# Performance work log

Measured on AMD Instinct MI355X. Metric: run time of the kernel, lower is better.

The kernel has to match this reference:

```python
import jax, jax.numpy as jnp
import numpy as np

# dims: batch, seq, state_dim, hidden, action_dim, layers, heads, bucket_size
B, T, SD, C, A, L, H, BS = 4, 4096, 256, 1024, 64, 6, 16, 64
HD = C // H
SCALE = 1.0 / np.sqrt(HD).astype(np.float32)
EPS = 1e-5


def _ln(x, w, b):
    m = jnp.mean(x, axis=-1, keepdims=True)
    v = jnp.var(x, axis=-1, keepdims=True)
    return (x - m) * jax.lax.rsqrt(v + EPS) * w + b


def _attn(x, qkv_w, qkv_b, out_w, out_b):
    # bucketed local attention: each bucket attends to itself + previous bucket (causal within own bucket)
    Bx, Tx, Cx = x.shape
    nb = Tx // BS
    qkv = x @ qkv_w + qkv_b                              # [B,T,3C]
    q, k, v = jnp.split(qkv, 3, axis=-1)
    bkt = lambda t: t.reshape(Bx, nb, BS, H, HD).transpose(0, 1, 3, 2, 4)  # [B,nb,H,BS,HD]
    qb, kb, vb = bkt(q), bkt(k), bkt(v)
    # previous bucket (first bucket's 'previous' is zeros), matching torch.roll + zeroing bucket 0
    kp = jnp.concatenate([jnp.zeros_like(kb[:, :1]), kb[:, :-1]], axis=1)
    vp = jnp.concatenate([jnp.zeros_like(vb[:, :1]), vb[:, :-1]], axis=1)
    kc = jnp.concatenate([kp, kb], axis=3)               # [B,nb,H,2BS,HD]
    vc = jnp.concatenate([vp, vb], axis=3)
    s = jnp.einsum('bnhid,bnhjd->bnhij', qb, kc) * SCALE # [B,nb,H,BS,2BS]
    i = jnp.arange(BS)[:, None]
    j = jnp.arange(2 * BS)[None, :]
    mask = (j < BS) | (j - BS <= i)
    s = jnp.where(mask, s, -jnp.inf)
    a = jax.nn.softmax(s, axis=-1)
    o = jnp.einsum('bnhij,bnhjd->bnhid', a, vc)          # [B,nb,H,BS,HD]
    o = o.transpose(0, 1, 3, 2, 4).reshape(Bx, Tx, Cx)
    return o @ out_w + out_b


def setup_inputs() -> dict:
    key = jax.random.key(0)
    ks = iter(jax.random.split(key, 40))
    rn = lambda shape, std=0.02: jax.random.normal(next(ks), shape, jnp.float32) * std
    return {
        'states': jax.random.normal(next(ks), (B, T, SD), jnp.float32),
        'state_embed_w': rn((SD, C)),
        'state_embed_b': jnp.zeros((C,), jnp.float32),
        'pos_embed': rn((1, T, C)),
        'ln1_w': jnp.ones((L, C), jnp.float32),
        'ln1_b': jnp.zeros((L, C), jnp.float32),
        'qkv_w': rn((L, C, 3 * C)),
        'qkv_b': jnp.zeros((L, 3 * C), jnp.float32),
        'attn_out_w': rn((L, C, C)),
        'attn_out_b': jnp.zeros((L, C), jnp.float32),
        'ln2_w': jnp.ones((L, C), jnp.float32),
        'ln2_b': jnp.zeros((L, C), jnp.float32),
        'mlp_w1': rn((L, C, 4 * C)),
        'mlp_b1': jnp.zeros((L, 4 * C), jnp.float32),
        'mlp_w2': rn((L, 4 * C, C)),
        'mlp_b2': jnp.zeros((L, C), jnp.float32),
        'lnf_w': jnp.ones((C,), jnp.float32),
        'lnf_b': jnp.zeros((C,), jnp.float32),
        'actor_w': rn((C, A)),
        'actor_b': jnp.zeros((A,), jnp.float32),
        'actor_logstd': jnp.zeros((1, A), jnp.float32),
        'critic_w': rn((C, 1)),
        'critic_b': jnp.zeros((1,), jnp.float32),
    }


def reference(states, state_embed_w, state_embed_b, pos_embed,
              ln1_w, ln1_b, qkv_w, qkv_b, attn_out_w, attn_out_b,
              ln2_w, ln2_b, mlp_w1, mlp_b1, mlp_w2, mlp_b2,
              lnf_w, lnf_b, actor_w, actor_b, actor_logstd, critic_w, critic_b):
    x = states @ state_embed_w + state_embed_b + pos_embed[:, :T]

    def step(x, p):
        l1w, l1b, qw, qb, ow, ob, l2w, l2b, w1, b1, w2, b2 = p
        x = x + _attn(_ln(x, l1w, l1b), qw, qb, ow, ob)
        h = _ln(x, l2w, l2b)
        x = x + (jax.nn.gelu(h @ w1 + b1, approximate=False) @ w2 + b2)
        return x, None

    blocks = (ln1_w, ln1_b, qkv_w, qkv_b, attn_out_w, attn_out_b,
              ln2_w, ln2_b, mlp_w1, mlp_b1, mlp_w2, mlp_b2)
    x, _ = jax.lax.scan(step, x, blocks)
    x = _ln(x, lnf_w, lnf_b)
    logits = x @ actor_w + actor_b          # [B,T,A]
    values = x @ critic_w + critic_b        # [B,T,1]
    return (logits, actor_logstd, values)
```

## Files before the change

### kernel.cpp

```cpp
#include <hip/hip_runtime.h>
#include <math.h>
#include <stdint.h>

#define T_SEQ 4096
#define CDIM  1024
#define NL    6
#define NH    16
#define BSZ   64
#define HDIM  64
#define MROWS 16384

typedef __bf16 bf16x8 __attribute__((ext_vector_type(8)));
typedef float  f32x4  __attribute__((ext_vector_type(4)));

__device__ __forceinline__ unsigned short f2bf(float f) {
  __bf16 h = (__bf16)f;
  return __builtin_bit_cast(unsigned short, h);
}
__device__ __forceinline__ float bf2f(unsigned short u) {
  unsigned int v = ((unsigned int)u) << 16;
  return __builtin_bit_cast(float, v);
}

typedef __attribute__((address_space(3))) unsigned int* lds_u32p;
typedef const __attribute__((address_space(1))) unsigned int* glb_u32p;
__device__ __forceinline__ void glds16(const void* g, void* l) {
  __builtin_amdgcn_global_load_lds((glb_u32p)(uintptr_t)g, (lds_u32p)(uintptr_t)l, 16, 0, 0);
}

__device__ __forceinline__ float erf_fast(float x) {
  float ax = fabsf(x);
  float t = __builtin_amdgcn_rcpf(fmaf(0.3275911f, ax, 1.0f));
  float y = t * fmaf(t, fmaf(t, fmaf(t, fmaf(t, 1.061405429f, -1.453152027f),
                                     1.421413741f), -0.284496736f), 0.254829592f);
  float r = 1.0f - y * __expf(-ax * ax);
  return copysignf(r, x);
}
__device__ __forceinline__ float gelu_fast(float v) {
  return 0.5f * v * (1.0f + erf_fast(v * 0.70710678118654752440f));
}

template<int OBF>
__global__ __launch_bounds__(256) void ln_kernel(const float* __restrict__ x,
    const float* __restrict__ w, const float* __restrict__ bb, void* __restrict__ out)
{
  int row = blockIdx.x;
  int tid = threadIdx.x;
  float4 v = ((const float4*)(x + (size_t)row * CDIM))[tid];
  float s  = v.x + v.y + v.z + v.w;
  float ss = v.x*v.x + v.y*v.y + v.z*v.z + v.w*v.w;
  #pragma unroll
  for (int o = 32; o > 0; o >>= 1) { s += __shfl_down(s, o); ss += __shfl_down(ss, o); }
  __shared__ float red[8];
  int wid = tid >> 6, lane = tid & 63;
  if (lane == 0) { red[wid] = s; red[4 + wid] = ss; }
  __syncthreads();
  if (tid == 0) {
    red[0] = red[0] + red[1] + red[2] + red[3];
    red[4] = red[4] + red[5] + red[6] + red[7];
  }
  __syncthreads();
  float mean = red[0] * (1.0f / CDIM);
  float var  = red[4] * (1.0f / CDIM) - mean * mean;
  float inv  = 1.0f / sqrtf(var + 1e-5f);
  float4 w4 = ((const float4*)w)[tid];
  float4 b4 = ((const float4*)bb)[tid];
  float4 o4;
  o4.x = (v.x - mean) * inv * w4.x + b4.x;
  o4.y = (v.y - mean) * inv * w4.y + b4.y;
  o4.z = (v.z - mean) * inv * w4.z + b4.z;
  o4.w = (v.w - mean) * inv * w4.w + b4.w;
  if (OBF) {
    ushort4 o;
    o.x = f2bf(o4.x); o.y = f2bf(o4.y); o.z = f2bf(o4.z); o.w = f2bf(o4.w);
    ((ushort4*)((unsigned short*)out + (size_t)row * CDIM))[tid] = o;
  } else {
    ((float4*)((float*)out + (size_t)row * CDIM))[tid] = o4;
  }
}

__global__ __launch_bounds__(256) void convT(const float* __restrict__ W,
    unsigned short* __restrict__ Wt, int K, int N)
{
  __shared__ float tile[32][33];
  const int kt = blockIdx.y * 32, nt = blockIdx.x * 32;
  const int r = threadIdx.x >> 3;
  const int c = (threadIdx.x & 7) * 4;
  float4 v = *(const float4*)(W + (size_t)(kt + r) * N + nt + c);
  tile[r][c] = v.x; tile[r][c+1] = v.y; tile[r][c+2] = v.z; tile[r][c+3] = v.w;
  __syncthreads();
  ushort4 o;
  o.x = f2bf(tile[c+0][r]); o.y = f2bf(tile[c+1][r]);
  o.z = f2bf(tile[c+2][r]); o.w = f2bf(tile[c+3][r]);
  *(ushort4*)(Wt + (size_t)(nt + r) * K + kt + c) = o;
}

__global__ void conv_flat(const float* __restrict__ in, unsigned short* __restrict__ out)
{
  int i = blockIdx.x * blockDim.x + threadIdx.x;
  float4 v = ((const float4*)in)[i];
  ushort4 o;
  o.x = f2bf(v.x); o.y = f2bf(v.y); o.z = f2bf(v.z); o.w = f2bf(v.w);
  ((ushort4*)out)[i] = o;
}

#define EPAD 68
#define GTILE 65536
template<int EPI, int OBF>
__global__ __launch_bounds__(512, 2) void gemm_bf16(
    const unsigned short* __restrict__ A, const unsigned short* __restrict__ Bt,
    const float* __restrict__ bias, const float* __restrict__ extra,
    void* __restrict__ Cout, int M, int N, int K)
{
  __shared__ __align__(16) char smem[2 * GTILE];
  const int tid = threadIdx.x;
  const int wave = tid >> 6, lane = tid & 63;
  const int ln15 = lane & 15, quad = lane >> 4;

  const int ntiles = N >> 8;
  const int per = ntiles << 3;
  const int g = blockIdx.x / per, rr = blockIdx.x % per;
  const int m0 = ((g << 3) + (rr & 7)) << 8;
  const int n0 = (rr >> 3) << 8;
  const int wm = (wave >> 2) * 128, wn = (wave & 3) * 64;

  const int srow = lane >> 3;
  const int scol = ((lane & 7) ^ srow) << 4;
  const size_t rs = (size_t)K * 2;
  const char* aSrc = (const char*)(A + (size_t)(m0 + wave * 8 + srow) * K) + scol;
  const char* bSrc = (const char*)(Bt + (size_t)(n0 + wave * 8 + srow) * K) + scol;
  const int sdst = wave * 1024;

  const int axor = (ln15 & 7) << 4;
  const int kq0 = (quad * 16) ^ axor;
  const int kq1 = (64 + quad * 16) ^ axor;
  const int aRd = (wm + ln15) * 128;
  const int bRd = (wn + ln15) * 128;

  f32x4 acc[8][4];
  #pragma unroll
  for (int i = 0; i < 8; ++i)
    #pragma unroll
    for (int j = 0; j < 4; ++j) acc[i][j] = (f32x4){0.f, 0.f, 0.f, 0.f};

  bf16x8 af[4][2];
  bf16x8 bfr[4][2];

  #define STAGE_A(buf, kt2) { \
    const char* s_ = aSrc + (size_t)(kt2) * 128; \
    char* d_ = smem + (buf) * GTILE + sdst; \
    glds16(s_,             d_); \
    glds16(s_ +  64 * rs,  d_ + 8192); \
    glds16(s_ + 128 * rs,  d_ + 16384); \
    glds16(s_ + 192 * rs,  d_ + 24576); }
  #define STAGE_B(buf, kt2) { \
    const char* s_ = bSrc + (size_t)(kt2) * 128; \
    char* d_ = smem + (buf) * GTILE + 32768 + sdst; \
    glds16(s_,             d_); \
    glds16(s_ +  64 * rs,  d_ + 8192); \
    glds16(s_ + 128 * rs,  d_ + 16384); \
    glds16(s_ + 192 * rs,  d_ + 24576); }
  #define LDA(buf, mh) { \
    const char* p_ = smem + (buf) * GTILE + aRd + (mh) * 8192; \
    _Pragma("unroll") \
    for (int mf = 0; mf < 4; ++mf) { \
      af[mf][0] = *(const bf16x8*)(p_ + mf * 2048 + kq0); \
      af[mf][1] = *(const bf16x8*)(p_ + mf * 2048 + kq1); } }
  #define LDB(buf, nh) { \
    const char* p_ = smem + (buf) * GTILE + 32768 + bRd + (nh) * 4096; \
    _Pragma("unroll") \
    for (int nf = 0; nf < 2; ++nf) { \
      bfr[(nh)*2+nf][0] = *(const bf16x8*)(p_ + nf * 2048 + kq0); \
      bfr[(nh)*2+nf][1] = *(const bf16x8*)(p_ + nf * 2048 + kq1); } }
  #define MMA(mh, nh) { \
    _Pragma("unroll") \
    for (int mf = 0; mf < 4; ++mf) \
      _Pragma("unroll") \
      for (int nf = 0; nf < 2; ++nf) { \
        acc[(mh)*4+mf][(nh)*2+nf] = __builtin_amdgcn_mfma_f32_16x16x32_bf16( \
            af[mf][0], bfr[(nh)*2+nf][0], acc[(mh)*4+mf][(nh)*2+nf], 0, 0, 0); \
        acc[(mh)*4+mf][(nh)*2+nf] = __builtin_amdgcn_mfma_f32_16x16x32_bf16( \
            af[mf][1], bfr[(nh)*2+nf][1], acc[(mh)*4+mf][(nh)*2+nf], 0, 0, 0); } }
  #define WAIT_LGKM do { asm volatile("s_waitcnt lgkmcnt(0)" ::: "memory"); \
                         __builtin_amdgcn_sched_barrier(0); } while (0)

  const int KT = K >> 6;
  STAGE_A(0, 0); STAGE_B(0, 0);
  asm volatile("s_waitcnt vmcnt(0)" ::: "memory");
  __builtin_amdgcn_s_barrier();

  int cur = 0;
  for (int kt = 0; kt < KT; ++kt) {
    const int nxt = cur ^ 1;
    const bool pf = (kt + 1 < KT);
    LDA(cur, 0); LDB(cur, 0);
    if (pf) STAGE_A(nxt, kt + 1);
    __builtin_amdgcn_s_barrier();
    WAIT_LGKM;
    __builtin_amdgcn_s_setprio(1);
    MMA(0, 0);
    __builtin_amdgcn_s_setprio(0);
    __builtin_amdgcn_s_barrier();
    LDB(cur, 1);
    if (pf) STAGE_B(nxt, kt + 1);
    __builtin_amdgcn_s_barrier();
    WAIT_LGKM;
    __builtin_amdgcn_s_setprio(1);
    MMA(0, 1);
    __builtin_amdgcn_s_setprio(0);
    __builtin_amdgcn_s_barrier();
    LDA(cur, 1);
    __builtin_amdgcn_s_barrier();
    WAIT_LGKM;
    __builtin_amdgcn_s_setprio(1);
    MMA(1, 0);
    __builtin_amdgcn_s_setprio(0);
    __builtin_amdgcn_s_barrier();
    __builtin_amdgcn_s_setprio(1);
    MMA(1, 1);
    __builtin_amdgcn_s_setprio(0);
    asm volatile("s_waitcnt vmcnt(0)" ::: "memory");
    __builtin_amdgcn_s_barrier();
    cur = nxt;
  }

  __builtin_amdgcn_s_barrier();
  float* ep = (float*)smem + wave * 16 * EPAD;
  const int cl = ln15, rq = quad * 4;
  #pragma unroll
  for (int i = 0; i < 8; ++i) {
    #pragma unroll
    for (int j = 0; j < 4; ++j) {
      const float bj = bias[n0 + wn + j * 16 + cl];
      #pragma unroll
      for (int r = 0; r < 4; ++r) {
        float val = acc[i][j][r] + bj;
        if (EPI == 2) val = gelu_fast(val);
        if (OBF) ((unsigned short*)ep)[(rq + r) * (2 * EPAD) + j * 16 + cl] = f2bf(val);
        else     ep[(rq + r) * EPAD + j * 16 + cl] = val;
      }
    }
    const int mbase = m0 + wm + i * 16;
    if (OBF) {
      #pragma unroll
      for (int s = 0; s < 2; ++s) {
        int f = s * 64 + lane;
        int row = f >> 3, ch = f & 7;
        uint4 v = *(const uint4*)((const unsigned short*)ep + row * (2 * EPAD) + ch * 8);
        *(uint4*)((unsigned short*)Cout + (size_t)(mbase + row) * N + n0 + wn + ch * 8) = v;
      }
    } else {
      #pragma unroll
      for (int s = 0; s < 4; ++s) {
        int f = s * 64 + lane;
        int row = f >> 4, ch = f & 15;
        float4 v = *(const float4*)(ep + row * EPAD + ch * 4);
        const int m = mbase + row;
        const size_t off = (size_t)m * N + n0 + wn + ch * 4;
        if (EPI == 1) {
          float4 e = *(const float4*)(extra + off);
          v.x += e.x; v.y += e.y; v.z += e.z; v.w += e.w;
        } else if (EPI == 3) {
          float4 e = *(const float4*)(extra + (size_t)(m & (T_SEQ - 1)) * N + n0 + wn + ch * 4);
          v.x += e.x; v.y += e.y; v.z += e.z; v.w += e.w;
        }
        *(float4*)((float*)Cout + off) = v;
      }
    }
  }
  #undef STAGE_A
  #undef STAGE_B
  #undef LDA
  #undef LDB
  #undef MMA
  #undef WAIT_LGKM
}

template<int EPI>
__global__ __launch_bounds__(256) void gemm_f32(const float* __restrict__ A,
    const float* __restrict__ B, const float* __restrict__ bias,
    const float* __restrict__ extra, float* __restrict__ C,
    int M, int N, int K)
{
  __shared__ float As[16][64];
  __shared__ float Bs[16][64];
  const int tid = threadIdx.x;
  const int m0 = blockIdx.x * 64, n0 = blockIdx.y * 64;
  const int tx = tid & 15, ty = tid >> 4;
  const int ar = tid >> 2, ak = (tid & 3) * 4;
  const int br = tid >> 4, bc = (tid & 15) * 4;
  const float* Ap = A + (size_t)(m0 + ar) * K + ak;
  const float* Bp = B + (size_t)br * N + n0 + bc;
  float acc[4][4] = {};
  for (int k0 = 0; k0 < K; k0 += 16) {
    float4 av = *(const float4*)(Ap + k0);
    float4 bv = *(const float4*)(Bp + (size_t)k0 * N);
    __syncthreads();
    As[ak+0][ar] = av.x; As[ak+1][ar] = av.y; As[ak+2][ar] = av.z; As[ak+3][ar] = av.w;
    *(float4*)&Bs[br][bc] = bv;
    __syncthreads();
    #pragma unroll
    for (int k = 0; k < 16; ++k) {
      float4 a4 = *(const float4*)&As[k][ty * 4];
      float4 b4 = *(const float4*)&Bs[k][tx * 4];
      float avv[4] = {a4.x, a4.y, a4.z, a4.w};
      float bvv[4] = {b4.x, b4.y, b4.z, b4.w};
      #pragma unroll
      for (int i = 0; i < 4; ++i)
        #pragma unroll
        for (int j = 0; j < 4; ++j)
          acc[i][j] = fmaf(avv[i], bvv[j], acc[i][j]);
    }
  }
  float4 bi = *(const float4*)(bias + n0 + tx * 4);
  #pragma unroll
  for (int i = 0; i < 4; ++i) {
    int m = m0 + ty * 4 + i;
    size_t off = (size_t)m * N + n0 + tx * 4;
    float4 r;
    r.x = acc[i][0] + bi.x; r.y = acc[i][1] + bi.y;
    r.z = acc[i][2] + bi.z; r.w = acc[i][3] + bi.w;
    if (EPI == 1) {
      float4 rs = *(const float4*)(extra + off);
      r.x += rs.x; r.y += rs.y; r.z += rs.z; r.w += rs.w;
    }
    *(float4*)(C + off) = r;
  }
}

#define ATT_KP 72
#define ATT_VP 136
__global__ __launch_bounds__(256) void attn_mfma(const unsigned short* __restrict__ qkv,
    unsigned short* __restrict__ out)
{
  __shared__ __align__(16) unsigned short Kb[128 * ATT_KP];
  __shared__ __align__(16) unsigned short Vt[64 * ATT_VP];
  __shared__ __align__(16) unsigned short Pb[64 * ATT_VP];
  const int n = blockIdx.x, h = blockIdx.y, b = blockIdx.z;
  const int tid = threadIdx.x;
  const int wave = tid >> 6, lane = tid & 63;
  const int ln15 = lane & 15, quad = lane >> 4;
  const int C3 = 3 * CDIM;
  const size_t bbase = (size_t)b * T_SEQ * C3;
  const int kcol = CDIM + h * HDIM, vcol = 2 * CDIM + h * HDIM;

  #pragma unroll
  for (int i = 0; i < 4; ++i) {
    int idx = tid + 256 * i;
    int j = idx >> 3, d8 = (idx & 7) * 8;
    uint4 r = make_uint4(0u, 0u, 0u, 0u);
    if (j >= 64 || n > 0) {
      int t = (j >= 64) ? (n * BSZ + j - 64) : ((n - 1) * BSZ + j);
      r = *(const uint4*)(qkv + bbase + (size_t)t * C3 + kcol + d8);
    }
    *(uint4*)&Kb[j * ATT_KP + d8] = r;
  }
  #pragma unroll
  for (int i = 0; i < 16; ++i) {
    int idx = tid + 256 * i;
    int j = idx >> 5, d2 = (idx & 31) * 2;
    unsigned int r = 0u;
    if (j >= 64 || n > 0) {
      int t = (j >= 64) ? (n * BSZ + j - 64) : ((n - 1) * BSZ + j);
      r = *(const unsigned int*)(qkv + bbase + (size_t)t * C3 + vcol + d2);
    }
    Vt[d2 * ATT_VP + j]       = (unsigned short)(r & 0xffffu);
    Vt[(d2 + 1) * ATT_VP + j] = (unsigned short)(r >> 16);
  }
  const int it = wave;
  const int qm = n * BSZ + it * 16 + ln15;
  bf16x8 aq[2];
  #pragma unroll
  for (int ks = 0; ks < 2; ++ks)
    aq[ks] = *(const bf16x8*)(qkv + bbase + (size_t)qm * C3 + h * HDIM + ks * 32 + quad * 8);
  __syncthreads();

  f32x4 accs[8];
  #pragma unroll
  for (int jt = 0; jt < 8; ++jt) accs[jt] = (f32x4){0.f, 0.f, 0.f, 0.f};
  #pragma unroll
  for (int jt = 0; jt < 8; ++jt)
    #pragma unroll
    for (int ks = 0; ks < 2; ++ks) {
      bf16x8 bk = *(const bf16x8*)&Kb[(jt * 16 + ln15) * ATT_KP + ks * 32 + quad * 8];
      accs[jt] = __builtin_amdgcn_mfma_f32_16x16x32_bf16(aq[ks], bk, accs[jt], 0, 0, 0);
    }

  #pragma unroll
  for (int r = 0; r < 4; ++r) {
    const int irow = it * 16 + quad * 4 + r;
    float p8[8];
    float mx = -1e30f;
    #pragma unroll
    for (int jt = 0; jt < 8; ++jt) {
      int j = jt * 16 + ln15;
      float s = accs[jt][r] * 0.125f;
      bool ok = (j < BSZ) || (j - BSZ <= irow);
      s = ok ? s : -1e30f;
      p8[jt] = s;
      mx = fmaxf(mx, s);
    }
    mx = fmaxf(mx, __shfl_xor(mx, 1));
    mx = fmaxf(mx, __shfl_xor(mx, 2));
    mx = fmaxf(mx, __shfl_xor(mx, 4));
    mx = fmaxf(mx, __shfl_xor(mx, 8));
    float l = 0.f;
    #pragma unroll
    for (int jt = 0; jt < 8; ++jt) { float e = __expf(p8[jt] - mx); p8[jt] = e; l += e; }
    l += __shfl_xor(l, 1); l += __shfl_xor(l, 2);
    l += __shfl_xor(l, 4); l += __shfl_xor(l, 8);
    const float linv = 1.0f / l;
    #pragma unroll
    for (int jt = 0; jt < 8; ++jt)
      Pb[irow * ATT_VP + jt * 16 + ln15] = f2bf(p8[jt] * linv);
  }

  f32x4 acco[4];
  #pragma unroll
  for (int dt = 0; dt < 4; ++dt) acco[dt] = (f32x4){0.f, 0.f, 0.f, 0.f};
  #pragma unroll
  for (int ks = 0; ks < 4; ++ks) {
    bf16x8 pa = *(const bf16x8*)&Pb[(it * 16 + ln15) * ATT_VP + ks * 32 + quad * 8];
    #pragma unroll
    for (int dt = 0; dt < 4; ++dt) {
      bf16x8 bv = *(const bf16x8*)&Vt[(dt * 16 + ln15) * ATT_VP + ks * 32 + quad * 8];
      acco[dt] = __builtin_amdgcn_mfma_f32_16x16x32_bf16(pa, bv, acco[dt], 0, 0, 0);
    }
  }

  unsigned short* op = out + (size_t)(b * T_SEQ + n * BSZ) * CDIM + h * HDIM;
  #pragma unroll
  for (int dt = 0; dt < 4; ++dt)
    #pragma unroll
    for (int r = 0; r < 4; ++r)
      op[(size_t)(it * 16 + quad * 4 + r) * CDIM + dt * 16 + ln15] = f2bf(acco[dt][r]);
}

__global__ __launch_bounds__(256) void critic_kernel(const float* __restrict__ x,
    const float* __restrict__ w, const float* __restrict__ b, float* __restrict__ out)
{
  int row = blockIdx.x * 4 + (threadIdx.x >> 6);
  int lane = threadIdx.x & 63;
  const float* xr = x + (size_t)row * CDIM;
  float s = 0.f;
  #pragma unroll
  for (int i = 0; i < 16; ++i) s = fmaf(xr[lane + 64*i], w[lane + 64*i], s);
  #pragma unroll
  for (int o = 32; o > 0; o >>= 1) s += __shfl_down(s, o);
  if (lane == 0) out[row] = s + b[0];
}

__global__ void copy64_kernel(const float* __restrict__ in, float* __restrict__ out)
{
  out[threadIdx.x] = in[threadIdx.x];
}

extern "C" void kernel_launch(void* const* d_in, const int* in_sizes, int n_in,
                              void* d_out, int out_size, void* d_ws, size_t ws_size,
                              hipStream_t stream)
{
  const float* states   = (const float*)d_in[0];
  const float* emb_w    = (const float*)d_in[1];
  const float* emb_b    = (const float*)d_in[2];
  const float* pos      = (const float*)d_in[3];
  const float* ln1_w    = (const float*)d_in[4];
  const float* ln1_b    = (const float*)d_in[5];
  const float* qkv_w    = (const float*)d_in[6];
  const float* qkv_b    = (const float*)d_in[7];
  const float* ow       = (const float*)d_in[8];
  const float* obs      = (const float*)d_in[9];
  const float* ln2_w    = (const float*)d_in[10];
  const float* ln2_b    = (const float*)d_in[11];
  const float* w1       = (const float*)d_in[12];
  const float* b1       = (const float*)d_in[13];
  const float* w2       = (const float*)d_in[14];
  const float* b2       = (const float*)d_in[15];
  const float* lnf_w    = (const float*)d_in[16];
  const float* lnf_b    = (const float*)d_in[17];
  const float* actor_w  = (const float*)d_in[18];
  const float* actor_b  = (const float*)d_in[19];
  const float* logstd   = (const float*)d_in[20];
  const float* critic_w = (const float*)d_in[21];
  const float* critic_b = (const float*)d_in[22];

  char* wsb = (char*)d_ws;
  float* x              = (float*)wsb;
  unsigned short* qkvb  = (unsigned short*)(wsb + (64ull  << 20));
  float* hbuf           = (float*)(wsb + (64ull << 20));
  unsigned short* lnb   = (unsigned short*)(wsb + (160ull << 20));
  unsigned short* mlpb  = (unsigned short*)(wsb + (192ull << 20));
  unsigned short* statesb = mlpb;
  unsigned short* wq    = (unsigned short*)(wsb + (320ull << 20));
  unsigned short* wo    = wq  + (size_t)3072 * 1024;
  unsigned short* wm1   = wo  + (size_t)1024 * 1024;
  unsigned short* wm2   = wm1 + (size_t)4096 * 1024;
  unsigned short* wemb  = wm2 + (size_t)1024 * 4096;

  float* logits     = (float*)d_out;
  float* out_logstd = logits + (size_t)MROWS * 64;
  float* out_values = out_logstd + 64;

  dim3 blk(256);
  dim3 gblk(512);

  conv_flat<<<4096, blk, 0, stream>>>(states, statesb);
  convT<<<dim3(1024/32, 256/32), blk, 0, stream>>>(emb_w, wemb, 256, 1024);
  gemm_bf16<3,0><<<dim3(64 * 4), gblk, 0, stream>>>(
      statesb, wemb, emb_b, pos, x, MROWS, CDIM, 256);

  for (int l = 0; l < NL; ++l) {
    convT<<<dim3(3072/32, 1024/32), blk, 0, stream>>>(qkv_w + (size_t)l*CDIM*3*CDIM, wq,  1024, 3072);
    convT<<<dim3(1024/32, 1024/32), blk, 0, stream>>>(ow    + (size_t)l*CDIM*CDIM,   wo,  1024, 1024);
    convT<<<dim3(4096/32, 1024/32), blk, 0, stream>>>(w1    + (size_t)l*CDIM*4*CDIM, wm1, 1024, 4096);
    convT<<<dim3(1024/32, 4096/32), blk, 0, stream>>>(w2    + (size_t)l*4*CDIM*CDIM, wm2, 4096, 1024);

    ln_kernel<1><<<MROWS, blk, 0, stream>>>(x, ln1_w + l*CDIM, ln1_b + l*CDIM, lnb);
    gemm_bf16<0,1><<<dim3(64 * 12), gblk, 0, stream>>>(
        lnb, wq, qkv_b + (size_t)l*3*CDIM, nullptr, qkvb, MROWS, 3*CDIM, CDIM);
    attn_mfma<<<dim3(T_SEQ/BSZ, NH, 4), blk, 0, stream>>>(qkvb, lnb);
    gemm_bf16<1,0><<<dim3(64 * 4), gblk, 0, stream>>>(
        lnb, wo, obs + (size_t)l*CDIM, x, x, MROWS, CDIM, CDIM);
    ln_kernel<1><<<MROWS, blk, 0, stream>>>(x, ln2_w + l*CDIM, ln2_b + l*CDIM, lnb);
    gemm_bf16<2,1><<<dim3(64 * 16), gblk, 0, stream>>>(
        lnb, wm1, b1 + (size_t)l*4*CDIM, nullptr, mlpb, MROWS, 4*CDIM, CDIM);
    gemm_bf16<1,0><<<dim3(64 * 4), gblk, 0, stream>>>(
        mlpb, wm2, b2 + (size_t)l*CDIM, x, x, MROWS, CDIM, 4*CDIM);
  }

  ln_kernel<0><<<MROWS, blk, 0, stream>>>(x, lnf_w, lnf_b, hbuf);
  gemm_f32<0><<<dim3(MROWS/64, 1), blk, 0, stream>>>(
      hbuf, actor_w, actor_b, nullptr, logits, MROWS, 64, CDIM);
  critic_kernel<<<MROWS/4, blk, 0, stream>>>(hbuf, critic_w, critic_b, out_values);
  copy64_kernel<<<1, 64, 0, stream>>>(logstd, out_logstd);
}
```

Baseline: 3.559 ms.

## Restructure bf16 GEMM LDS layout into K-halves with finer vmcnt waits

```diff
diff --git a/kernel.cpp b/kernel.cpp
--- a/kernel.cpp
+++ b/kernel.cpp
@@ -124,18 +124,16 @@
   const int n0 = (rr >> 3) << 8;
   const int wm = (wave >> 2) * 128, wn = (wave & 3) * 64;
 
-  const int srow = lane >> 3;
-  const int scol = ((lane & 7) ^ srow) << 4;
-  const size_t rs = (size_t)K * 2;
-  const char* aSrc = (const char*)(A + (size_t)(m0 + wave * 8 + srow) * K) + scol;
-  const char* bSrc = (const char*)(Bt + (size_t)(n0 + wave * 8 + srow) * K) + scol;
-  const int sdst = wave * 1024;
-
-  const int axor = (ln15 & 7) << 4;
-  const int kq0 = (quad * 16) ^ axor;
-  const int kq1 = (64 + quad * 16) ^ axor;
-  const int aRd = (wm + ln15) * 128;
-  const int bRd = (wn + ln15) * 128;
+  const int srow16 = lane >> 2;
+  const int scol   = (((lane & 3) ^ (srow16 & 3)) << 4);
+  const char* aS0 = (const char*)(A  + (size_t)(m0 + wave * 32 + srow16) * K) + scol;
+  const char* aS1 = aS0 + (size_t)16 * K * 2;
+  const char* bS0 = (const char*)(Bt + (size_t)(n0 + wave * 32 + srow16) * K) + scol;
+  const char* bS1 = bS0 + (size_t)16 * K * 2;
+
+  const int xorc = ((quad ^ (ln15 & 3)) << 4);
+  const int aRd = (wm + ln15) * 64 + xorc;
+  const int bRd = 32768 + (wn + ln15) * 64 + xorc;
 
   f32x4 acc[8][4];
   #pragma unroll
@@ -143,83 +141,82 @@
     #pragma unroll
     for (int j = 0; j < 4; ++j) acc[i][j] = (f32x4){0.f, 0.f, 0.f, 0.f};
 
-  bf16x8 af[4][2];
-  bf16x8 bfr[4][2];
-
-  #define STAGE_A(buf, kt2) { \
-    const char* s_ = aSrc + (size_t)(kt2) * 128; \
-    char* d_ = smem + (buf) * GTILE + sdst; \
-    glds16(s_,             d_); \
-    glds16(s_ +  64 * rs,  d_ + 8192); \
-    glds16(s_ + 128 * rs,  d_ + 16384); \
-    glds16(s_ + 192 * rs,  d_ + 24576); }
-  #define STAGE_B(buf, kt2) { \
-    const char* s_ = bSrc + (size_t)(kt2) * 128; \
-    char* d_ = smem + (buf) * GTILE + 32768 + sdst; \
-    glds16(s_,             d_); \
-    glds16(s_ +  64 * rs,  d_ + 8192); \
-    glds16(s_ + 128 * rs,  d_ + 16384); \
-    glds16(s_ + 192 * rs,  d_ + 24576); }
-  #define LDA(buf, mh) { \
-    const char* p_ = smem + (buf) * GTILE + aRd + (mh) * 8192; \
-    _Pragma("unroll") \
-    for (int mf = 0; mf < 4; ++mf) { \
-      af[mf][0] = *(const bf16x8*)(p_ + mf * 2048 + kq0); \
-      af[mf][1] = *(const bf16x8*)(p_ + mf * 2048 + kq1); } }
-  #define LDB(buf, nh) { \
-    const char* p_ = smem + (buf) * GTILE + 32768 + bRd + (nh) * 4096; \
-    _Pragma("unroll") \
-    for (int nf = 0; nf < 2; ++nf) { \
-      bfr[(nh)*2+nf][0] = *(const bf16x8*)(p_ + nf * 2048 + kq0); \
-      bfr[(nh)*2+nf][1] = *(const bf16x8*)(p_ + nf * 2048 + kq1); } }
-  #define MMA(mh, nh) { \
+  bf16x8 af[4];
+  bf16x8 bfr[4];
+
+  #define STAGE(buf, kt2, kh) { \
+    const size_t ko_ = (size_t)(kt2) * 128 + (size_t)(kh) * 64; \
+    char* da_ = smem + (buf) * GTILE + (kh) * 16384 + wave * 2048; \
+    char* db_ = da_ + 32768; \
+    glds16(aS0 + ko_, da_); \
+    glds16(aS1 + ko_, da_ + 1024); \
+    glds16(bS0 + ko_, db_); \
+    glds16(bS1 + ko_, db_ + 1024); }
+  #define LDA(buf, mh, ks) { \
+    const char* p_ = smem + (buf) * GTILE + (ks) * 16384 + (mh) * 4096 + aRd; \
+    af[0] = *(const bf16x8*)(p_); \
+    af[1] = *(const bf16x8*)(p_ + 1024); \
+    af[2] = *(const bf16x8*)(p_ + 2048); \
+    af[3] = *(const bf16x8*)(p_ + 3072); }
+  #define LDB(buf, ks) { \
+    const char* p_ = smem + (buf) * GTILE + (ks) * 16384 + bRd; \
+    bfr[0] = *(const bf16x8*)(p_); \
+    bfr[1] = *(const bf16x8*)(p_ + 1024); \
+    bfr[2] = *(const bf16x8*)(p_ + 2048); \
+    bfr[3] = *(const bf16x8*)(p_ + 3072); }
+  #define MMA(mh) { \
     _Pragma("unroll") \
     for (int mf = 0; mf < 4; ++mf) \
       _Pragma("unroll") \
-      for (int nf = 0; nf < 2; ++nf) { \
-        acc[(mh)*4+mf][(nh)*2+nf] = __builtin_amdgcn_mfma_f32_16x16x32_bf16( \
-            af[mf][0], bfr[(nh)*2+nf][0], acc[(mh)*4+mf][(nh)*2+nf], 0, 0, 0); \
-        acc[(mh)*4+mf][(nh)*2+nf] = __builtin_amdgcn_mfma_f32_16x16x32_bf16( \
-            af[mf][1], bfr[(nh)*2+nf][1], acc[(mh)*4+mf][(nh)*2+nf], 0, 0, 0); } }
+      for (int nf = 0; nf < 4; ++nf) \
+        acc[(mh) * 4 + mf][nf] = __builtin_amdgcn_mfma_f32_16x16x32_bf16( \
+            af[mf], bfr[nf], acc[(mh) * 4 + mf][nf], 0, 0, 0); }
   #define WAIT_LGKM do { asm volatile("s_waitcnt lgkmcnt(0)" ::: "memory"); \
                          __builtin_amdgcn_sched_barrier(0); } while (0)
+  #define WAIT_VM(n) do { asm volatile("s_waitcnt vmcnt(" #n ")" ::: "memory"); \
+                          __builtin_amdgcn_sched_barrier(0); } while (0)
 
   const int KT = K >> 6;
-  STAGE_A(0, 0); STAGE_B(0, 0);
-  asm volatile("s_waitcnt vmcnt(0)" ::: "memory");
+  STAGE(0, 0, 0);
+  STAGE(0, 0, 1);
+  WAIT_VM(4);
   __builtin_amdgcn_s_barrier();
 
   int cur = 0;
   for (int kt = 0; kt < KT; ++kt) {
     const int nxt = cur ^ 1;
     const bool pf = (kt + 1 < KT);
-    LDA(cur, 0); LDB(cur, 0);
-    if (pf) STAGE_A(nxt, kt + 1);
+    LDA(cur, 0, 0); LDB(cur, 0);
+    if (pf) STAGE(nxt, kt + 1, 0);
     __builtin_amdgcn_s_barrier();
     WAIT_LGKM;
     __builtin_amdgcn_s_setprio(1);
-    MMA(0, 0);
+    MMA(0);
     __builtin_amdgcn_s_setprio(0);
     __builtin_amdgcn_s_barrier();
-    LDB(cur, 1);
-    if (pf) STAGE_B(nxt, kt + 1);
+    LDA(cur, 1, 0);
+    if (pf) STAGE(nxt, kt + 1, 1);
     __builtin_amdgcn_s_barrier();
     WAIT_LGKM;
     __builtin_amdgcn_s_setprio(1);
-    MMA(0, 1);
+    MMA(1);
     __builtin_amdgcn_s_setprio(0);
-    __builtin_amdgcn_s_barrier();
-    LDA(cur, 1);
+    if (pf) WAIT_VM(8); else WAIT_VM(0);
+    __builtin_amdgcn_s_barrier();
+    LDA(cur, 0, 1); LDB(cur, 1);
     __builtin_amdgcn_s_barrier();
     WAIT_LGKM;
     __builtin_amdgcn_s_setprio(1);
-    MMA(1, 0);
+    MMA(0);
     __builtin_amdgcn_s_setprio(0);
     __builtin_amdgcn_s_barrier();
+    LDA(cur, 1, 1);
+    __builtin_amdgcn_s_barrier();
+    WAIT_LGKM;
     __builtin_amdgcn_s_setprio(1);
-    MMA(1, 1);
+    MMA(1);
     __builtin_amdgcn_s_setprio(0);
-    asm volatile("s_waitcnt vmcnt(0)" ::: "memory");
+    if (pf) WAIT_VM(4);
     __builtin_amdgcn_s_barrier();
     cur = nxt;
   }
@@ -240,7 +237,7 @@
         else     ep[(rq + r) * EPAD + j * 16 + cl] = val;
       }
     }
-    const int mbase = m0 + wm + i * 16;
+    const int mbase = m0 + wm + ((i >> 2) * 64) + ((i & 3) * 16);
     if (OBF) {
       #pragma unroll
       for (int s = 0; s < 2; ++s) {
@@ -268,12 +265,12 @@
       }
     }
   }
-  #undef STAGE_A
-  #undef STAGE_B
+  #undef STAGE
   #undef LDA
   #undef LDB
   #undef MMA
   #undef WAIT_LGKM
+  #undef WAIT_VM
 }
 
 template<int EPI>
```

New measurement: 4.108 ms. 1.15x slower.
